# Optimization experiments

Measured on AMD Instinct MI355X. Metric: run time of the kernel, lower is better.

## Reference

```python
import jax, jax.numpy as jnp
import numpy as np

B, LQ, LKV, D, H = 2, 2048, 4096, 1024, 16
HD = D // H  # 64


def setup_inputs() -> dict:
    key = jax.random.key(0)
    ks = jax.random.split(key, 12)
    s = 1.0 / np.sqrt(D)
    return {
        "x_q": jax.random.normal(ks[0], (B, LQ, D), jnp.float32),
        "x_kv": jax.random.normal(ks[1], (B, LKV, D), jnp.float32),
        "mask_kv": jax.random.randint(ks[2], (B, LKV), 0, 2).astype(bool),
        "Wq": jax.random.normal(ks[3], (D, D), jnp.float32) * s,
        "bq": jnp.zeros((D,), jnp.float32),
        "Wk": jax.random.normal(ks[4], (D, D), jnp.float32) * s,
        "bk": jnp.zeros((D,), jnp.float32),
        "Wv": jax.random.normal(ks[5], (D, D), jnp.float32) * s,
        "bv": jnp.zeros((D,), jnp.float32),
        "Wo": jax.random.normal(ks[6], (D, D), jnp.float32) * s,
        "bo": jnp.zeros((D,), jnp.float32),
    }


def reference(x_q, x_kv, mask_kv, Wq, bq, Wk, bk, Wv, bv, Wo, bo):
    Bq, Lq, _ = x_q.shape
    Lkv = x_kv.shape[1]
    # projections (dropout=0.0 -> identity)
    q = (x_q @ Wq + bq).reshape(Bq, Lq, H, HD).transpose(0, 2, 1, 3)    # [B,H,Lq,hd]
    k = (x_kv @ Wk + bk).reshape(Bq, Lkv, H, HD).transpose(0, 2, 1, 3)  # [B,H,Lkv,hd]
    v = (x_kv @ Wv + bv).reshape(Bq, Lkv, H, HD).transpose(0, 2, 1, 3)  # [B,H,Lkv,hd]
    # scaled dot-product attention with kv masking
    logits = jnp.einsum("bhqd,bhkd->bhqk", q, k) / np.sqrt(HD)          # [B,H,Lq,Lkv]
    logits = jnp.where(mask_kv[:, None, None, :], logits, -jnp.inf)
    weights = jax.nn.softmax(logits, axis=-1)
    attn = jnp.einsum("bhqk,bhkd->bhqd", weights, v)                    # [B,H,Lq,hd]
    attn = attn.transpose(0, 2, 1, 3).reshape(Bq, Lq, D)
    return attn @ Wo + bo
```

## Files before the change

kernel.cpp:

```cpp
#include <hip/hip_runtime.h>
#include <hip/hip_bf16.h>

typedef unsigned short u16;
typedef unsigned int u32;
typedef __attribute__((ext_vector_type(8))) unsigned short u16x8;
typedef __attribute__((ext_vector_type(8))) short s16x8;
typedef __attribute__((ext_vector_type(4))) float f32x4;
typedef __attribute__((ext_vector_type(16))) float f32x16;

#define NB 2
#define NLQ 2048
#define NLKV 4096
#define ND 1024
#define NH 16
#define NHD 64
#define SCALE 0.125f
#define QSC (SCALE * 1.44269504f)

#define GL16(g, l)                                                            \
    __builtin_amdgcn_global_load_lds(                                         \
        (const __attribute__((address_space(1))) void*)(g),                   \
        (__attribute__((address_space(3))) void*)(l), 16, 0, 0)

__device__ __forceinline__ u16 f2bf(float f) {
    __hip_bfloat16 h = __float2bfloat16(f);
    return *(u16*)&h;
}

__device__ __forceinline__ float fast_exp2(float x) {
    float r;
    asm("v_exp_f32 %0, %1" : "=v"(r) : "v"(x));
    return r;
}

__device__ __forceinline__ u32 pkbf(float lo, float hi_) {
    u32 r;
    asm("v_cvt_pk_bf16_f32 %0, %1, %2" : "=v"(r) : "v"(lo), "v"(hi_));
    return r;
}

__device__ __forceinline__ void pl32swap(u32& a, u32& b) {
    asm("v_permlane32_swap_b32 %0, %1" : "+v"(a), "+v"(b));
}

__global__ __launch_bounds__(256) void prep_kernel(
    const float* __restrict__ xq, const float* __restrict__ xkv,
    const int* __restrict__ mask,
    const float* __restrict__ w0, const float* __restrict__ w1,
    const float* __restrict__ w2, const float* __restrict__ w3,
    u16* __restrict__ oq, u16* __restrict__ okv, u16* __restrict__ mbf,
    u16* __restrict__ o0, u16* __restrict__ o1,
    u16* __restrict__ o2, u16* __restrict__ o3) {
    __shared__ float t[32][33];
    const int bid = blockIdx.x;
    const int tid = threadIdx.x;
    if (bid < 6144) {
        const float* in;
        u16* out;
        int i0;
        if (bid < 2048) { in = xq; out = oq; i0 = bid; }
        else { in = xkv; out = okv; i0 = bid - 2048; }
        int i = i0 * 256 + tid;
        const float4* p = (const float4*)in;
        float4 a = p[2 * i], b = p[2 * i + 1];
        u16x8 o;
        o[0] = f2bf(a.x); o[1] = f2bf(a.y); o[2] = f2bf(a.z); o[3] = f2bf(a.w);
        o[4] = f2bf(b.x); o[5] = f2bf(b.y); o[6] = f2bf(b.z); o[7] = f2bf(b.w);
        ((u16x8*)out)[i] = o;
        return;
    }
    if (bid < 6176) {
        int g = (bid - 6144) * 256 + tid;
        mbf[g] = mask[g] ? 0x3F80 : 0;
        return;
    }
    int tb = bid - 6176;
    int z = tb >> 10;
    int rem = tb & 1023;
    int n0 = (rem & 31) * 32, k0 = (rem >> 5) * 32;
    const float* w = z == 0 ? w0 : z == 1 ? w1 : z == 2 ? w2 : w3;
    u16* o = z == 0 ? o0 : z == 1 ? o1 : z == 2 ? o2 : o3;
    int tx = tid & 31, ty = tid >> 5;
#pragma unroll
    for (int i = 0; i < 4; i++) t[ty + 8 * i][tx] = w[(k0 + ty + 8 * i) * ND + n0 + tx];
    __syncthreads();
#pragma unroll
    for (int i = 0; i < 4; i++) o[(n0 + ty + 8 * i) * ND + k0 + tx] = f2bf(t[tx][ty + 8 * i]);
}

__global__ __launch_bounds__(512) void qkv_kernel(
    const u16* __restrict__ xq, const u16* __restrict__ xkv,
    const u16* __restrict__ wq_t, const u16* __restrict__ wkv_t,
    const float* __restrict__ bq, const float* __restrict__ bk,
    const float* __restrict__ bv, const int* __restrict__ vmask,
    u16* __restrict__ Qh, u16* __restrict__ Kh, u16* __restrict__ VTh) {
    const int bid = blockIdx.x;
    const int swz = (bid & 7) * 160 + (bid >> 3);
    const bool isQ = swz < 256;
    int m0, n0;
    const u16 *A, *Bt;
    if (isQ) {
        m0 = (swz >> 3) * 128; n0 = (swz & 7) * 128;
        A = xq; Bt = wq_t;
    } else {
        int t2 = swz - 256;
        m0 = (t2 >> 4) * 128; n0 = (t2 & 15) * 128;
        A = xkv; Bt = wkv_t;
    }
    const bool isV = !isQ && n0 >= 1024;

    __shared__ __align__(16) u16 As[128 * 64];
    __shared__ __align__(16) u16 Bs[128 * 64];
    const int tid = threadIdx.x;
    const int lane = tid & 63, w = tid >> 6;
    const int wr = w >> 2, wc = w & 3;
    const int lr = lane & 15, lg = lane >> 4;
    const int l7 = lr & 7;

    f32x4 acc[4][2];
#pragma unroll
    for (int i = 0; i < 4; i++)
#pragma unroll
        for (int j = 0; j < 2; j++)
#pragma unroll
            for (int r = 0; r < 4; r++) acc[i][j][r] = 0.f;

    const int srow = tid >> 3, sj = tid & 7;
    const int sx8 = (sj ^ (srow & 7)) * 8;
    const u16* Ag1 = A + (size_t)(m0 + srow) * ND + sx8;
    const u16* Ag2 = A + (size_t)(m0 + 64 + srow) * ND + sx8;
    const u16* Bg1 = Bt + (size_t)(n0 + srow) * ND + sx8;
    const u16* Bg2 = Bt + (size_t)(n0 + 64 + srow) * ND + sx8;
    u16* lA1 = &As[w * 512];
    u16* lA2 = &As[4096 + w * 512];
    u16* lB1 = &Bs[w * 512];
    u16* lB2 = &Bs[4096 + w * 512];

    for (int kt = 0; kt < ND; kt += 64) {
        GL16(Ag1 + kt, lA1);
        GL16(Ag2 + kt, lA2);
        GL16(Bg1 + kt, lB1);
        GL16(Bg2 + kt, lB2);
        __syncthreads();

#pragma unroll
        for (int kk = 0; kk < 2; kk++) {
            const int slot = ((kk * 4 + lg) ^ l7) * 8;
            s16x8 af[4], bf[2];
#pragma unroll
            for (int i = 0; i < 4; i++)
                af[i] = *(const s16x8*)&As[(wr * 64 + i * 16 + lr) * 64 + slot];
#pragma unroll
            for (int j = 0; j < 2; j++)
                bf[j] = *(const s16x8*)&Bs[(wc * 32 + j * 16 + lr) * 64 + slot];
            if (isV) {
#pragma unroll
                for (int mi = 0; mi < 4; mi++)
#pragma unroll
                    for (int ni = 0; ni < 2; ni++)
                        acc[mi][ni] = __builtin_amdgcn_mfma_f32_16x16x32_bf16(
                            bf[ni], af[mi], acc[mi][ni], 0, 0, 0);
            } else {
#pragma unroll
                for (int mi = 0; mi < 4; mi++)
#pragma unroll
                    for (int ni = 0; ni < 2; ni++)
                        acc[mi][ni] = __builtin_amdgcn_mfma_f32_16x16x32_bf16(
                            af[mi], bf[ni], acc[mi][ni], 0, 0, 0);
            }
        }
        __syncthreads();
    }

#pragma unroll
    for (int mi = 0; mi < 4; mi++)
#pragma unroll
        for (int ni = 0; ni < 2; ni++)
#pragma unroll
            for (int r = 0; r < 4; r++) {
                if (isQ) {
                    int m = m0 + wr * 64 + mi * 16 + lg * 4 + r;
                    int n = n0 + wc * 32 + ni * 16 + lr;
                    int h = n >> 6, d = n & 63;
                    int b = m >> 11, lq = m & 2047;
                    Qh[((((size_t)b * NH + h) * NLQ + lq) << 6) + d] =
                        f2bf((acc[mi][ni][r] + bq[n]) * QSC);
                } else if (!isV) {
                    int m = m0 + wr * 64 + mi * 16 + lg * 4 + r;
                    int n = n0 + wc * 32 + ni * 16 + lr;
                    int h = n >> 6, d = n & 63;
                    int b = m >> 12, lkv = m & 4095;
                    Kh[((((size_t)b * NH + h) * NLKV + lkv) << 6) + d] =
                        f2bf(acc[mi][ni][r] + bk[n]);
                } else {
                    int n2 = (n0 - 1024) + wc * 32 + ni * 16 + lg * 4 + r;
                    int m = m0 + wr * 64 + mi * 16 + lr;
                    int h = n2 >> 6, d = n2 & 63;
                    int b = m >> 12, lkv = m & 4095;
                    float val = vmask[(size_t)b * NLKV + lkv]
                                    ? acc[mi][ni][r] + bv[n2] : 0.f;
                    VTh[(((size_t)b * NH + h) * NHD + d) * NLKV + lkv] = f2bf(val);
                }
            }
}

__global__ __launch_bounds__(256) void ogemm_kernel(
    const u16* __restrict__ A, const u16* __restrict__ Bt,
    const float* __restrict__ bias, float* __restrict__ Cout) {
    __shared__ __align__(16) u16 As[64 * 32];
    __shared__ __align__(16) u16 Bs[128 * 32];
    const int m0 = blockIdx.x * 64;
    const int n0 = blockIdx.y * 128;
    const int tid = threadIdx.x;
    const int lane = tid & 63, w = tid >> 6;
    const int wr = w >> 1, wc = w & 1;
    const int lr = lane & 15, lg = lane >> 4;
    const int ko = lg * 8;

    f32x4 acc[2][4];
#pragma unroll
    for (int i = 0; i < 2; i++)
#pragma unroll
        for (int j = 0; j < 4; j++)
#pragma unroll
            for (int r = 0; r < 4; r++) acc[i][j][r] = 0.f;

    const int srow = tid >> 2, spart = tid & 3;
    const u16* Ag = A + (size_t)(m0 + srow) * ND + spart * 8;
    const u16* Bg = Bt + (size_t)(n0 + srow) * ND + spart * 8;
    const u16* Bg2 = Bt + (size_t)(n0 + 64 + srow) * ND + spart * 8;
    u16* lA = &As[w * 512];
    u16* lB = &Bs[w * 512];
    u16* lB2 = &Bs[2048 + w * 512];

    for (int kt = 0; kt < ND; kt += 32) {
        GL16(Ag + kt, lA);
        GL16(Bg + kt, lB);
        GL16(Bg2 + kt, lB2);
        __syncthreads();

        s16x8 af[2], bf[4];
#pragma unroll
        for (int i = 0; i < 2; i++)
            af[i] = *(const s16x8*)&As[(wr * 32 + i * 16 + lr) * 32 + ko];
#pragma unroll
        for (int j = 0; j < 4; j++)
            bf[j] = *(const s16x8*)&Bs[(wc * 64 + j * 16 + lr) * 32 + ko];
#pragma unroll
        for (int mi = 0; mi < 2; mi++)
#pragma unroll
            for (int ni = 0; ni < 4; ni++)
                acc[mi][ni] = __builtin_amdgcn_mfma_f32_16x16x32_bf16(
                    af[mi], bf[ni], acc[mi][ni], 0, 0, 0);
        __syncthreads();
    }

#pragma unroll
    for (int mi = 0; mi < 2; mi++)
#pragma unroll
        for (int ni = 0; ni < 4; ni++)
#pragma unroll
            for (int r = 0; r < 4; r++) {
                int m = m0 + wr * 32 + mi * 16 + lg * 4 + r;
                int n = n0 + wc * 64 + ni * 16 + lr;
                Cout[(size_t)m * ND + n] = acc[mi][ni][r] + bias[n];
            }
}

__global__ __launch_bounds__(256) void attn_kernel(
    const u16* __restrict__ Qh, const u16* __restrict__ Kh,
    const u16* __restrict__ VTh, const u16* __restrict__ mbf,
    u16* __restrict__ attn) {
    const int l = blockIdx.x + 16 * blockIdx.y;
    const int qt = l >> 5;
    const int bh = (l & 7) * 4 + ((l >> 3) & 3);
    const int b = bh >> 4, h = bh & 15;
    const int tid = threadIdx.x;
    const int lane = tid & 63, w = tid >> 6;
    const int c = lane & 31, hi = lane >> 5;
    const int c7 = c & 7, c3 = (c >> 3) & 3;

    __shared__ __align__(16) u16 kt[2][4096];
    __shared__ __align__(16) u16 vt[2][4096];

    const int qw0 = qt * 128 + w * 32;
    const u16* Qb = Qh + (size_t)bh * NLQ * NHD;
    const u16* Kb = Kh + (size_t)bh * NLKV * NHD;
    const u16* VTb = VTh + (size_t)bh * NHD * NLKV;
    const u16* mbfb = mbf + (size_t)b * NLKV;

    s16x8 qa[4];
#pragma unroll
    for (int kb = 0; kb < 4; kb++)
        qa[kb] = *(const s16x8*)(Qb + (size_t)(qw0 + c) * NHD + kb * 16 + hi * 8);

    f32x16 o0, o1, lacc;
#pragma unroll
    for (int r = 0; r < 16; r++) { o0[r] = 0.f; o1[r] = 0.f; lacc[r] = 0.f; }

    const int srow = 8 * w + (lane >> 3);
    const int sj = lane & 7;
    const int sx8 = (sj ^ (srow & 7) ^ ((srow >> 3) & 3)) * 8;
    const u16* kS1 = Kb + (size_t)srow * NHD + sx8;
    const u16* kS2 = Kb + (size_t)(srow + 32) * NHD + sx8;
    const u16* vS1 = VTb + (size_t)srow * NLKV + sx8;
    const u16* vS2 = VTb + (size_t)(srow + 32) * NLKV + sx8;
    const int d1 = w * 512, d2 = 2048 + w * 512;

    GL16(kS1, &kt[0][d1]);
    GL16(kS2, &kt[0][d2]);
    GL16(vS1, &vt[0][d1]);
    GL16(vS2, &vt[0][d2]);

    const int NT = NLKV / 64;
    for (int t = 0; t < NT; t++) {
        const int cur = t & 1;
        __syncthreads();
        if (t + 1 < NT) {
            size_t kvo = (size_t)(t + 1) * 64;
            GL16(kS1 + kvo * NHD, &kt[cur ^ 1][d1]);
            GL16(kS2 + kvo * NHD, &kt[cur ^ 1][d2]);
            GL16(vS1 + kvo, &vt[cur ^ 1][d1]);
            GL16(vS2 + kvo, &vt[cur ^ 1][d2]);
        }
        s16x8 mf[4];
#pragma unroll
        for (int pb = 0; pb < 4; pb++)
            mf[pb] = *(const s16x8*)(mbfb + t * 64 + pb * 16 + hi * 8);

        const u16* ktc = kt[cur];
        const u16* vtc = vt[cur];

        f32x16 s0, s1;
#pragma unroll
        for (int r = 0; r < 16; r++) { s0[r] = 0.f; s1[r] = 0.f; }
        __builtin_amdgcn_s_setprio(1);
#pragma unroll
        for (int kb = 0; kb < 4; kb++) {
            int slot = ((kb * 2 + hi) ^ c7 ^ c3) << 3;
            s16x8 kf0 = *(const s16x8*)&ktc[c * 64 + slot];
            s16x8 kf1 = *(const s16x8*)&ktc[(32 + c) * 64 + slot];
            s0 = __builtin_amdgcn_mfma_f32_32x32x16_bf16(kf0, qa[kb], s0, 0, 0, 0);
            s1 = __builtin_amdgcn_mfma_f32_32x32x16_bf16(kf1, qa[kb], s1, 0, 0, 0);
        }
        __builtin_amdgcn_s_setprio(0);

        float p0a[16], p1a[16];
#pragma unroll
        for (int r = 0; r < 16; r++) {
            p0a[r] = fast_exp2(s0[r]);
            p1a[r] = fast_exp2(s1[r]);
        }

        u32 pka[8], pkb2[8];
#pragma unroll
        for (int i = 0; i < 8; i++) {
            pka[i] = pkbf(p0a[2 * i], p0a[2 * i + 1]);
            pkb2[i] = pkbf(p1a[2 * i], p1a[2 * i + 1]);
        }
        pl32swap(pka[0], pka[2]); pl32swap(pka[1], pka[3]);
        pl32swap(pka[4], pka[6]); pl32swap(pka[5], pka[7]);
        pl32swap(pkb2[0], pkb2[2]); pl32swap(pkb2[1], pkb2[3]);
        pl32swap(pkb2[4], pkb2[6]); pl32swap(pkb2[5], pkb2[7]);

        union { u32 u[4]; s16x8 h; } fr[4];
#pragma unroll
        for (int i = 0; i < 4; i++) {
            fr[0].u[i] = pka[i];
            fr[1].u[i] = pka[4 + i];
            fr[2].u[i] = pkb2[i];
            fr[3].u[i] = pkb2[4 + i];
        }

        __builtin_amdgcn_s_setprio(1);
#pragma unroll
        for (int pb = 0; pb < 4; pb++) {
            int slot = ((pb * 2 + hi) ^ c7 ^ c3) << 3;
            s16x8 vf0 = *(const s16x8*)&vtc[c * 64 + slot];
            s16x8 vf1 = *(const s16x8*)&vtc[(32 + c) * 64 + slot];
            o0 = __builtin_amdgcn_mfma_f32_32x32x16_bf16(vf0, fr[pb].h, o0, 0, 0, 0);
            o1 = __builtin_amdgcn_mfma_f32_32x32x16_bf16(vf1, fr[pb].h, o1, 0, 0, 0);
            lacc = __builtin_amdgcn_mfma_f32_32x32x16_bf16(mf[pb], fr[pb].h, lacc, 0, 0, 0);
        }
        __builtin_amdgcn_s_setprio(0);
    }

    float linv = 1.f / lacc[0];

    __syncthreads();
    u32* osh = (u32*)kt + w * 1024;
#pragma unroll
    for (int r = 0; r < 16; r += 2) {
        int d = (r & 3) + 8 * (r >> 2) + 4 * hi;
        u32 plo = pkbf(o0[r] * linv, o0[r + 1] * linv);
        u32 phi = pkbf(o1[r] * linv, o1[r + 1] * linv);
        int dc0 = d >> 1, dc1 = (d + 32) >> 1;
        osh[c * 32 + (((dc0 >> 2) ^ c7) << 2) + (dc0 & 3)] = plo;
        osh[c * 32 + (((dc1 >> 2) ^ c7) << 2) + (dc1 & 3)] = phi;
    }
    __syncthreads();
#pragma unroll
    for (int i = 0; i < 4; i++) {
        int row = 8 * i + (lane >> 3);
        int jj = lane & 7;
        u32 v0 = osh[row * 32 + ((jj ^ (row & 7)) << 2) + 0];
        u32 v1 = osh[row * 32 + ((jj ^ (row & 7)) << 2) + 1];
        u32 v2 = osh[row * 32 + ((jj ^ (row & 7)) << 2) + 2];
        u32 v3 = osh[row * 32 + ((jj ^ (row & 7)) << 2) + 3];
        u32* gp = (u32*)(attn + ((size_t)b * NLQ + qw0 + row) * ND + h * NHD + jj * 8);
        gp[0] = v0; gp[1] = v1; gp[2] = v2; gp[3] = v3;
    }
}

extern "C" void kernel_launch(void* const* d_in, const int* in_sizes, int n_in,
                              void* d_out, int out_size, void* d_ws, size_t ws_size,
                              hipStream_t stream) {
    const float* x_q = (const float*)d_in[0];
    const float* x_kv = (const float*)d_in[1];
    const int* mask = (const int*)d_in[2];
    const float* Wq = (const float*)d_in[3];
    const float* bq = (const float*)d_in[4];
    const float* Wk = (const float*)d_in[5];
    const float* bk = (const float*)d_in[6];
    const float* Wv = (const float*)d_in[7];
    const float* bv = (const float*)d_in[8];
    const float* Wo = (const float*)d_in[9];
    const float* bo = (const float*)d_in[10];
    float* out = (float*)d_out;

    size_t off = 0;
    auto carve = [&](size_t bytes) {
        void* p = (char*)d_ws + off;
        off += (bytes + 255) & ~(size_t)255;
        return p;
    };
    u16* xq_bf = (u16*)carve((size_t)NB * NLQ * ND * 2);
    u16* xkv_bf = (u16*)carve((size_t)NB * NLKV * ND * 2);
    u16* wq_t = (u16*)carve((size_t)ND * ND * 2);
    u16* wkv_t = (u16*)carve((size_t)2 * ND * ND * 2);
    u16* wo_t = (u16*)carve((size_t)ND * ND * 2);
    u16* Qh = (u16*)carve((size_t)NB * NH * NLQ * NHD * 2);
    u16* Kh = (u16*)carve((size_t)NB * NH * NLKV * NHD * 2);
    u16* VTh = (u16*)carve((size_t)NB * NH * NLKV * NHD * 2);
    u16* attn_bf = (u16*)carve((size_t)NB * NLQ * ND * 2);
    u16* mbfw = (u16*)carve((size_t)NB * NLKV * 2);

    prep_kernel<<<dim3(10272), 256, 0, stream>>>(
        x_q, x_kv, mask, Wq, Wk, Wv, Wo,
        xq_bf, xkv_bf, mbfw, wq_t, wkv_t, wkv_t + (size_t)ND * ND, wo_t);
    qkv_kernel<<<dim3(1280), 512, 0, stream>>>(xq_bf, xkv_bf, wq_t, wkv_t,
                                               bq, bk, bv, mask, Qh, Kh, VTh);
    attn_kernel<<<dim3(16, 32), 256, 0, stream>>>(Qh, Kh, VTh, mbfw, attn_bf);
    ogemm_kernel<<<dim3(64, 8), 256, 0, stream>>>(attn_bf, wo_t, bo, out);
}
```

Before: 200.2 us.

## Widen output GEMM K-tile to 64 with XOR swizzle; split attention exp/PV into halves

The output projection GEMM now stages 64-wide K tiles per iteration instead of 32, with an XOR swizzle on the LDS column layout to avoid bank conflicts. This halves the number of barrier pairs and adds more loads in flight. In the attention kernel, the exp/pack/PV-MFMA sequence is split into two halves (s0 then s1), so the first half's MFMAs can start while the second half's exponentials compute, and fewer registers are live at once. The cost is double the LDS in the GEMM and possibly different compiler scheduling.

```diff
diff --git a/kernel.cpp b/kernel.cpp
--- a/kernel.cpp
+++ b/kernel.cpp
@@ -207,15 +207,15 @@
 __global__ __launch_bounds__(256) void ogemm_kernel(
     const u16* __restrict__ A, const u16* __restrict__ Bt,
     const float* __restrict__ bias, float* __restrict__ Cout) {
-    __shared__ __align__(16) u16 As[64 * 32];
-    __shared__ __align__(16) u16 Bs[128 * 32];
+    __shared__ __align__(16) u16 As[64 * 64];
+    __shared__ __align__(16) u16 Bs[128 * 64];
     const int m0 = blockIdx.x * 64;
     const int n0 = blockIdx.y * 128;
     const int tid = threadIdx.x;
     const int lane = tid & 63, w = tid >> 6;
     const int wr = w >> 1, wc = w & 1;
     const int lr = lane & 15, lg = lane >> 4;
-    const int ko = lg * 8;
+    const int l7 = lr & 7;
 
     f32x4 acc[2][4];
 #pragma unroll
@@ -225,33 +225,47 @@
 #pragma unroll
             for (int r = 0; r < 4; r++) acc[i][j][r] = 0.f;
 
-    const int srow = tid >> 2, spart = tid & 3;
-    const u16* Ag = A + (size_t)(m0 + srow) * ND + spart * 8;
-    const u16* Bg = Bt + (size_t)(n0 + srow) * ND + spart * 8;
-    const u16* Bg2 = Bt + (size_t)(n0 + 64 + srow) * ND + spart * 8;
-    u16* lA = &As[w * 512];
-    u16* lB = &Bs[w * 512];
+    const int srow = tid >> 3, sj = tid & 7;
+    const int sx8 = (sj ^ (srow & 7)) * 8;
+    const u16* Ag1 = A + (size_t)(m0 + srow) * ND + sx8;
+    const u16* Ag2 = A + (size_t)(m0 + 32 + srow) * ND + sx8;
+    const u16* Bg1 = Bt + (size_t)(n0 + srow) * ND + sx8;
+    const u16* Bg2 = Bt + (size_t)(n0 + 32 + srow) * ND + sx8;
+    const u16* Bg3 = Bt + (size_t)(n0 + 64 + srow) * ND + sx8;
+    const u16* Bg4 = Bt + (size_t)(n0 + 96 + srow) * ND + sx8;
+    u16* lA1 = &As[w * 512];
+    u16* lA2 = &As[2048 + w * 512];
+    u16* lB1 = &Bs[w * 512];
     u16* lB2 = &Bs[2048 + w * 512];
-
-    for (int kt = 0; kt < ND; kt += 32) {
-        GL16(Ag + kt, lA);
-        GL16(Bg + kt, lB);
+    u16* lB3 = &Bs[4096 + w * 512];
+    u16* lB4 = &Bs[6144 + w * 512];
+
+    for (int kt = 0; kt < ND; kt += 64) {
+        GL16(Ag1 + kt, lA1);
+        GL16(Ag2 + kt, lA2);
+        GL16(Bg1 + kt, lB1);
         GL16(Bg2 + kt, lB2);
+        GL16(Bg3 + kt, lB3);
+        GL16(Bg4 + kt, lB4);
         __syncthreads();
 
-        s16x8 af[2], bf[4];
-#pragma unroll
-        for (int i = 0; i < 2; i++)
-            af[i] = *(const s16x8*)&As[(wr * 32 + i * 16 + lr) * 32 + ko];
-#pragma unroll
-        for (int j = 0; j < 4; j++)
-            bf[j] = *(const s16x8*)&Bs[(wc * 64 + j * 16 + lr) * 32 + ko];
-#pragma unroll
-        for (int mi = 0; mi < 2; mi++)
-#pragma unroll
-            for (int ni = 0; ni < 4; ni++)
-                acc[mi][ni] = __builtin_amdgcn_mfma_f32_16x16x32_bf16(
-                    af[mi], bf[ni], acc[mi][ni], 0, 0, 0);
+#pragma unroll
+        for (int kk = 0; kk < 2; kk++) {
+            const int slot = ((kk * 4 + lg) ^ l7) * 8;
+            s16x8 af[2], bf[4];
+#pragma unroll
+            for (int i = 0; i < 2; i++)
+                af[i] = *(const s16x8*)&As[(wr * 32 + i * 16 + lr) * 64 + slot];
+#pragma unroll
+            for (int j = 0; j < 4; j++)
+                bf[j] = *(const s16x8*)&Bs[(wc * 64 + j * 16 + lr) * 64 + slot];
+#pragma unroll
+            for (int mi = 0; mi < 2; mi++)
+#pragma unroll
+                for (int ni = 0; ni < 4; ni++)
+                    acc[mi][ni] = __builtin_amdgcn_mfma_f32_16x16x32_bf16(
+                        af[mi], bf[ni], acc[mi][ni], 0, 0, 0);
+        }
         __syncthreads();
     }
 
@@ -345,44 +359,61 @@
         }
         __builtin_amdgcn_s_setprio(0);
 
-        float p0a[16], p1a[16];
-#pragma unroll
-        for (int r = 0; r < 16; r++) {
-            p0a[r] = fast_exp2(s0[r]);
-            p1a[r] = fast_exp2(s1[r]);
-        }
-
-        u32 pka[8], pkb2[8];
-#pragma unroll
-        for (int i = 0; i < 8; i++) {
-            pka[i] = pkbf(p0a[2 * i], p0a[2 * i + 1]);
-            pkb2[i] = pkbf(p1a[2 * i], p1a[2 * i + 1]);
-        }
-        pl32swap(pka[0], pka[2]); pl32swap(pka[1], pka[3]);
-        pl32swap(pka[4], pka[6]); pl32swap(pka[5], pka[7]);
-        pl32swap(pkb2[0], pkb2[2]); pl32swap(pkb2[1], pkb2[3]);
-        pl32swap(pkb2[4], pkb2[6]); pl32swap(pkb2[5], pkb2[7]);
-
-        union { u32 u[4]; s16x8 h; } fr[4];
-#pragma unroll
-        for (int i = 0; i < 4; i++) {
-            fr[0].u[i] = pka[i];
-            fr[1].u[i] = pka[4 + i];
-            fr[2].u[i] = pkb2[i];
-            fr[3].u[i] = pkb2[4 + i];
-        }
-
-        __builtin_amdgcn_s_setprio(1);
-#pragma unroll
-        for (int pb = 0; pb < 4; pb++) {
-            int slot = ((pb * 2 + hi) ^ c7 ^ c3) << 3;
-            s16x8 vf0 = *(const s16x8*)&vtc[c * 64 + slot];
-            s16x8 vf1 = *(const s16x8*)&vtc[(32 + c) * 64 + slot];
-            o0 = __builtin_amdgcn_mfma_f32_32x32x16_bf16(vf0, fr[pb].h, o0, 0, 0, 0);
-            o1 = __builtin_amdgcn_mfma_f32_32x32x16_bf16(vf1, fr[pb].h, o1, 0, 0, 0);
-            lacc = __builtin_amdgcn_mfma_f32_32x32x16_bf16(mf[pb], fr[pb].h, lacc, 0, 0, 0);
-        }
-        __builtin_amdgcn_s_setprio(0);
+        {
+            float p0a[16];
+#pragma unroll
+            for (int r = 0; r < 16; r++) p0a[r] = fast_exp2(s0[r]);
+            u32 pka[8];
+#pragma unroll
+            for (int i = 0; i < 8; i++) pka[i] = pkbf(p0a[2 * i], p0a[2 * i + 1]);
+            pl32swap(pka[0], pka[2]); pl32swap(pka[1], pka[3]);
+            pl32swap(pka[4], pka[6]); pl32swap(pka[5], pka[7]);
+            union { u32 u[4]; s16x8 h; } fr[2];
+#pragma unroll
+            for (int i = 0; i < 4; i++) {
+                fr[0].u[i] = pka[i];
+                fr[1].u[i] = pka[4 + i];
+            }
+            __builtin_amdgcn_s_setprio(1);
+#pragma unroll
+            for (int pb = 0; pb < 2; pb++) {
+                int slot = ((pb * 2 + hi) ^ c7 ^ c3) << 3;
+                s16x8 vf0 = *(const s16x8*)&vtc[c * 64 + slot];
+                s16x8 vf1 = *(const s16x8*)&vtc[(32 + c) * 64 + slot];
+                o0 = __builtin_amdgcn_mfma_f32_32x32x16_bf16(vf0, fr[pb].h, o0, 0, 0, 0);
+                o1 = __builtin_amdgcn_mfma_f32_32x32x16_bf16(vf1, fr[pb].h, o1, 0, 0, 0);
+                lacc = __builtin_amdgcn_mfma_f32_32x32x16_bf16(mf[pb], fr[pb].h, lacc, 0, 0, 0);
+            }
+            __builtin_amdgcn_s_setprio(0);
+        }
+
+        {
+            float p1a[16];
+#pragma unroll
+            for (int r = 0; r < 16; r++) p1a[r] = fast_exp2(s1[r]);
+            u32 pkb2[8];
+#pragma unroll
+            for (int i = 0; i < 8; i++) pkb2[i] = pkbf(p1a[2 * i], p1a[2 * i + 1]);
+            pl32swap(pkb2[0], pkb2[2]); pl32swap(pkb2[1], pkb2[3]);
+            pl32swap(pkb2[4], pkb2[6]); pl32swap(pkb2[5], pkb2[7]);
+            union { u32 u[4]; s16x8 h; } fr[2];
+#pragma unroll
+            for (int i = 0; i < 4; i++) {
+                fr[0].u[i] = pkb2[i];
+                fr[1].u[i] = pkb2[4 + i];
+            }
+            __builtin_amdgcn_s_setprio(1);
+#pragma unroll
+            for (int pb = 0; pb < 2; pb++) {
+                int slot = (((pb + 2) * 2 + hi) ^ c7 ^ c3) << 3;
+                s16x8 vf0 = *(const s16x8*)&vtc[c * 64 + slot];
+                s16x8 vf1 = *(const s16x8*)&vtc[(32 + c) * 64 + slot];
+                o0 = __builtin_amdgcn_mfma_f32_32x32x16_bf16(vf0, fr[pb].h, o0, 0, 0, 0);
+                o1 = __builtin_amdgcn_mfma_f32_32x32x16_bf16(vf1, fr[pb].h, o1, 0, 0, 0);
+                lacc = __builtin_amdgcn_mfma_f32_32x32x16_bf16(mf[pb + 2], fr[pb].h, lacc, 0, 0, 0);
+            }
+            __builtin_amdgcn_s_setprio(0);
+        }
     }
 
     float linv = 1.f / lacc[0];
```

Measured after the change: 199.5 us. No clear change (-0.4%).
